# Optimization experiments

Measured on AMD Instinct MI355X. Metric: run time of the kernel, lower is better.

## Reference

```python
import jax, jax.numpy as jnp
import numpy as np

B, LBL, T = 128, 1024, 255  # batch, label_size, max_num_trials


def setup_inputs() -> dict:
    key = jax.random.key(0)
    k1, k2, k3 = jax.random.split(key, 3)
    inp = jax.random.normal(k1, (B, LBL), dtype=jnp.float32)
    target = jax.random.randint(k2, (B, LBL), 0, 2, dtype=jnp.int32)  # binary multi-label
    u = jax.random.uniform(k3, (B, LBL, T), dtype=jnp.float32)  # per-(i,j,trial) sampling noise
    return {"input": inp, "u": u, "target": target}


def reference(input, u, target):
    b, lbl = input.shape
    t = u.shape[-1]  # max_num_trials

    # rank_weights: rw[0]=1, rw[i]=rw[i-1] + (1/i + 1)
    i = jnp.arange(lbl, dtype=jnp.float32)
    incr = jnp.where(i == 0, 1.0, 1.0 + 1.0 / jnp.maximum(i, 1.0))
    rank_weights = jnp.cumsum(incr)  # [LBL]

    pos = (target > 0).astype(input.dtype)
    neg = (target == 0).astype(input.dtype)

    # uniform sampling among negative labels of each row (with replacement across trials,
    # matching np.random.choice of a single element per trial)
    n_neg = jnp.sum(target == 0, axis=1)  # [B] int32
    order = jnp.argsort(target, axis=1)  # stable: zeros (negatives) first, original order
    k = (u * n_neg[:, None, None].astype(u.dtype)).astype(jnp.int32)
    k = jnp.minimum(k, jnp.maximum(n_neg - 1, 0)[:, None, None])  # [B,LBL,T]
    neg_idx = jnp.take_along_axis(order, k.reshape(b, lbl * t), axis=1)  # [B, LBL*T]
    sampled = jnp.take_along_axis(input, neg_idx, axis=1).reshape(b, lbl, t)

    margin = sampled - input[:, :, None]  # [B,LBL,T]
    success = margin >= 0  # loop exits when sample_score_margin >= 0
    any_success = jnp.any(success, axis=-1)
    first_success = jnp.argmax(success, axis=-1)  # first trial index with margin >= 0
    num_trials = jnp.where(any_success, first_success + 1, t)  # [B,LBL]

    r_j = t // num_trials  # floor(max_num_trials / num_trials)
    L = jnp.where(target == 1, rank_weights[r_j], 0.0)  # only rows where target==1

    # sum_k (1 - pos*input + neg*input), dim=1 keepdim
    margin_term = jnp.sum(1.0 - pos * input + neg * input, axis=1, keepdims=True)  # [B,1]
    loss = jnp.sum(L * margin_term, axis=1)  # [B]
    return jnp.sum(loss, axis=0)  # scalar
```

## Files before the change

### kernel.cpp

```cpp
#include <hip/hip_runtime.h>

#define BB   128
#define LBL  1024
#define TT   255
#define CH   8
#define NTHREADS 256

__global__ __launch_bounds__(NTHREADS) void warp_loss_kernel(
    const float* __restrict__ input,
    const float* __restrict__ u,
    const int*   __restrict__ target,
    float* __restrict__ out)
{
    __shared__ float         s_input[LBL];
    __shared__ float         s_negscore[LBL];
    __shared__ unsigned char s_target[LBL];
    __shared__ float         s_rw[256];
    __shared__ float         s_wavesum[NTHREADS / 64];
    __shared__ int           s_nneg;
    __shared__ float         s_margin;

    const int b    = blockIdx.x;
    const int ch   = blockIdx.y;
    const int tid  = threadIdx.x;
    const int lane = tid & 63;
    const int wv   = tid >> 6;

    const float* inrow = input  + (size_t)b * LBL;
    const int*   tgrow = target + (size_t)b * LBL;
    float rin[LBL / NTHREADS];
    int   rtg[LBL / NTHREADS];
#pragma unroll
    for (int i = 0; i < LBL / NTHREADS; ++i) {
        int j = tid + i * NTHREADS;
        rin[i] = inrow[j];
        rtg[i] = tgrow[j];
    }

    {
        double h = 0.0;
        for (int k = 1; k <= tid; ++k) h += 1.0 / (double)k;
        s_rw[tid] = (float)(1.0 + (double)tid + h);
    }

#pragma unroll
    for (int i = 0; i < LBL / NTHREADS; ++i) {
        int j = tid + i * NTHREADS;
        s_input[j]  = rin[i];
        s_target[j] = (unsigned char)(rtg[i] != 0);
    }
    __syncthreads();

    if (wv == 0) {
        int base = 0;
        for (int it = 0; it < LBL / 64; ++it) {
            int j = it * 64 + lane;
            bool isneg = (s_target[j] == 0);
            unsigned long long m = __ballot(isneg);
            int pfx = __popcll(m & ((1ull << lane) - 1ull));
            if (isneg) s_negscore[base + pfx] = s_input[j];
            base += __popcll(m);
        }
        if (lane == 0) {
            s_nneg = base;
            if (base == 0) s_negscore[0] = s_input[0];
        }
    }
    if (wv == 1) {
        float acc = 0.f;
        for (int j = lane; j < LBL; j += 64) {
            float x = s_input[j];
            acc += 1.0f + (s_target[j] ? -x : x);
        }
#pragma unroll
        for (int off = 32; off > 0; off >>= 1) acc += __shfl_down(acc, off, 64);
        if (lane == 0) s_margin = acc;
    }
    __syncthreads();

    const int   nneg  = s_nneg;
    const float nnegf = (float)nneg;
    const int   kmax  = nneg > 0 ? nneg - 1 : 0;

    float Lsum = 0.f;
    const int WPR  = CH * (NTHREADS / 64);
    const int wrow = ch * (NTHREADS / 64) + wv;
    for (int j = wrow; j < LBL; j += WPR) {
        if (!s_target[j]) continue;
        const float score = s_input[j];
        const float* urow = u + ((size_t)b * LBL + j) * TT;
        int num_trials = TT;
#pragma unroll 1
        for (int t0 = 0; t0 < TT; t0 += 64) {
            int t = t0 + lane;
            bool ok = false;
            if (t < TT) {
                float uv = urow[t];
                int k = (int)(uv * nnegf);
                k = k < kmax ? k : kmax;
                ok = (s_negscore[k] >= score);
            }
            unsigned long long m = __ballot(ok);
            if (m) { num_trials = t0 + __ffsll(m); break; }
        }
        int r = TT / num_trials;
        Lsum += s_rw[r];
    }

    if (lane == 0) s_wavesum[wv] = Lsum;
    __syncthreads();
    if (tid == 0) {
        float tot = 0.f;
#pragma unroll
        for (int w = 0; w < NTHREADS / 64; ++w) tot += s_wavesum[w];
        atomicAdd(out, tot * s_margin);
    }
}

extern "C" void kernel_launch(void* const* d_in, const int* in_sizes, int n_in,
                              void* d_out, int out_size, void* d_ws, size_t ws_size,
                              hipStream_t stream) {
    const float* input  = (const float*)d_in[0];
    const float* u      = (const float*)d_in[1];
    const int*   target = (const int*)d_in[2];
    float* out = (float*)d_out;

    hipMemsetAsync(out, 0, sizeof(float) * out_size, stream);

    dim3 grid(BB, CH);
    warp_loss_kernel<<<grid, NTHREADS, 0, stream>>>(input, u, target, out);
}
```

Baseline: 212.5 us.

## Prefetch first u chunk for all rows and scan-compute rank weights

The per-thread serial double-precision harmonic sum is replaced by a parallel prefix scan in shared memory, which removes a long per-thread loop (up to 255 iterations in thread 255). The first 64 trials of u for every positive row a wave owns are loaded up front, before the negative compaction, so those global loads overlap the setup work instead of being issued serially per row. Rows whose first 64 trials all fail fall back to the old sequential loop. The trade-offs are more registers spent on the prefetched values and rank weights summed in float rather than double.

New measurement: 186.6 us. 12.2% less time.

```diff
diff --git a/kernel.cpp b/kernel.cpp
--- a/kernel.cpp
+++ b/kernel.cpp
@@ -5,6 +5,9 @@
 #define TT   255
 #define CH   8
 #define NTHREADS 256
+#define NWAVES (NTHREADS / 64)
+#define WPR  (CH * NWAVES)
+#define LPW  (LBL / WPR)
 
 __global__ __launch_bounds__(NTHREADS) void warp_loss_kernel(
     const float* __restrict__ input,
@@ -15,8 +18,8 @@
     __shared__ float         s_input[LBL];
     __shared__ float         s_negscore[LBL];
     __shared__ unsigned char s_target[LBL];
-    __shared__ float         s_rw[256];
-    __shared__ float         s_wavesum[NTHREADS / 64];
+    __shared__ float         s_rw[NTHREADS];
+    __shared__ float         s_wavesum[NWAVES];
     __shared__ int           s_nneg;
     __shared__ float         s_margin;
 
@@ -37,10 +40,14 @@
         rtg[i] = tgrow[j];
     }
 
-    {
-        double h = 0.0;
-        for (int k = 1; k <= tid; ++k) h += 1.0 / (double)k;
-        s_rw[tid] = (float)(1.0 + (double)tid + h);
+    s_rw[tid] = (tid == 0) ? 1.0f : 1.0f + 1.0f / (float)tid;
+    __syncthreads();
+#pragma unroll
+    for (int off = 1; off < NTHREADS; off <<= 1) {
+        float add = (tid >= off) ? s_rw[tid - off] : 0.0f;
+        __syncthreads();
+        s_rw[tid] += add;
+        __syncthreads();
     }
 
 #pragma unroll
@@ -50,6 +57,22 @@
         s_target[j] = (unsigned char)(rtg[i] != 0);
     }
     __syncthreads();
+
+    const int wrow = ch * NWAVES + wv;
+    unsigned long long pm;
+    {
+        bool p = (lane < LPW) && (s_target[wrow + lane * WPR] != 0);
+        pm = __ballot(p);
+    }
+    const float* ubase = u + (size_t)b * LBL * TT;
+    float uv[LPW];
+#pragma unroll
+    for (int i = 0; i < LPW; ++i) {
+        if ((pm >> i) & 1) {
+            int j = wrow + i * WPR;
+            uv[i] = ubase[(size_t)j * TT + lane];
+        }
+    }
 
     if (wv == 0) {
         int base = 0;
@@ -83,28 +106,35 @@
     const int   kmax  = nneg > 0 ? nneg - 1 : 0;
 
     float Lsum = 0.f;
-    const int WPR  = CH * (NTHREADS / 64);
-    const int wrow = ch * (NTHREADS / 64) + wv;
-    for (int j = wrow; j < LBL; j += WPR) {
-        if (!s_target[j]) continue;
+#pragma unroll
+    for (int i = 0; i < LPW; ++i) {
+        if (!((pm >> i) & 1)) continue;
+        const int   j     = wrow + i * WPR;
         const float score = s_input[j];
-        const float* urow = u + ((size_t)b * LBL + j) * TT;
-        int num_trials = TT;
+        int k = (int)(uv[i] * nnegf);
+        k = k < kmax ? k : kmax;
+        bool ok = (s_negscore[k] >= score);
+        unsigned long long m = __ballot(ok);
+        int num_trials;
+        if (m) {
+            num_trials = __ffsll(m);
+        } else {
+            num_trials = TT;
 #pragma unroll 1
-        for (int t0 = 0; t0 < TT; t0 += 64) {
-            int t = t0 + lane;
-            bool ok = false;
-            if (t < TT) {
-                float uv = urow[t];
-                int k = (int)(uv * nnegf);
-                k = k < kmax ? k : kmax;
-                ok = (s_negscore[k] >= score);
+            for (int t0 = 64; t0 < TT; t0 += 64) {
+                int t = t0 + lane;
+                bool ok2 = false;
+                if (t < TT) {
+                    float uvv = ubase[(size_t)j * TT + t];
+                    int kk = (int)(uvv * nnegf);
+                    kk = kk < kmax ? kk : kmax;
+                    ok2 = (s_negscore[kk] >= score);
+                }
+                unsigned long long m2 = __ballot(ok2);
+                if (m2) { num_trials = t0 + __ffsll(m2); break; }
             }
-            unsigned long long m = __ballot(ok);
-            if (m) { num_trials = t0 + __ffsll(m); break; }
         }
-        int r = TT / num_trials;
-        Lsum += s_rw[r];
+        Lsum += s_rw[TT / num_trials];
     }
 
     if (lane == 0) s_wavesum[wv] = Lsum;
@@ -112,7 +142,7 @@
     if (tid == 0) {
         float tot = 0.f;
 #pragma unroll
-        for (int w = 0; w < NTHREADS / 64; ++w) tot += s_wavesum[w];
+        for (int w = 0; w < NWAVES; ++w) tot += s_wavesum[w];
         atomicAdd(out, tot * s_margin);
     }
 }
```
